# Performance work log

Measured on AMD Instinct MI355X. Metric: run time of the kernel, lower is better.

Reference implementation:

```python
import jax, jax.numpy as jnp
import numpy as np

B, S, E_BERT = 64, 512, 768
H = 64        # GRU hidden per direction (hidden_dim=128 bidirectional)
T = 16        # num output tags
P = 32        # pos_num_tags = attention embed dim


def setup_inputs() -> dict:
    key = jax.random.key(0)
    ks = jax.random.split(key, 20)
    def n(k, shape, s=0.1):
        return jax.random.normal(k, shape, dtype=jnp.float32) * s
    return {
        "bert_embed": n(ks[0], (B, S, E_BERT), 1.0),
        "input2": n(ks[1], (B, S, P), 1.0),
        "targets": jax.random.randint(ks[2], (B, S), 0, T),
        # forward-direction GRU (torch layout: W_ih (3H,E), W_hh (3H,H))
        "Wih_f": n(ks[3], (3 * H, E_BERT)), "Whh_f": n(ks[4], (3 * H, H)),
        "bih_f": n(ks[5], (3 * H,)), "bhh_f": n(ks[6], (3 * H,)),
        # backward-direction GRU
        "Wih_b": n(ks[7], (3 * H, E_BERT)), "Whh_b": n(ks[8], (3 * H, H)),
        "bih_b": n(ks[9], (3 * H,)), "bhh_b": n(ks[10], (3 * H,)),
        # dense (no bias): (2H -> T)
        "Wdense": n(ks[11], (2 * H, T)),
        # single-head MultiheadAttention over pos features
        "in_proj_w": n(ks[12], (3 * P, P)), "in_proj_b": n(ks[13], (3 * P,)),
        "out_proj_w": n(ks[14], (P, P)), "out_proj_b": n(ks[15], (P,)),
        # fusion linear (no bias): (T+P -> T)
        "Wfuse": n(ks[16], (T + P, T)),
        # CRF params
        "crf_start": n(ks[17], (T,)), "crf_end": n(ks[18], (T,)),
        "crf_trans": n(ks[19], (T, T)),
    }


def _gru_dir(x, Wih, Whh, bih, bhh, reverse):
    # x: (B,S,E) -> outputs (B,S,H); torch GRU cell math.
    xp = jnp.einsum('bse,ge->bsg', x, Wih) + bih      # precompute input gates (B,S,3H)
    xp = jnp.swapaxes(xp, 0, 1)                        # (S,B,3H)
    h0 = jnp.zeros((x.shape[0], Whh.shape[1]), x.dtype)
    def step(h, xt):
        gh = h @ Whh.T + bhh
        xr, xz, xn = jnp.split(xt, 3, axis=-1)
        hr, hz, hn = jnp.split(gh, 3, axis=-1)
        r = jax.nn.sigmoid(xr + hr)
        z = jax.nn.sigmoid(xz + hz)
        nw = jnp.tanh(xn + r * hn)
        h = (1.0 - z) * nw + z * h
        return h, h
    _, ys = jax.lax.scan(step, h0, xp, reverse=reverse)
    return jnp.swapaxes(ys, 0, 1)                      # (B,S,H)


def _forward(bert_embed, input2, targets,
             Wih_f, Whh_f, bih_f, bhh_f,
             Wih_b, Whh_b, bih_b, bhh_b,
             Wdense, in_proj_w, in_proj_b, out_proj_w, out_proj_b,
             Wfuse, crf_start, crf_end, crf_trans):
    # Bi-GRU over frozen BERT embeddings
    fwd = _gru_dir(bert_embed, Wih_f, Whh_f, bih_f, bhh_f, False)
    bwd = _gru_dir(bert_embed, Wih_b, Whh_b, bih_b, bhh_b, True)
    lstm_out = jnp.concatenate([fwd, bwd], axis=-1)    # (B,S,2H)
    dense = lstm_out @ Wdense                          # (B,S,T)

    # single-head self-attention on POS features (torch MultiheadAttention)
    qkv = input2 @ in_proj_w.T + in_proj_b
    q, k, v = jnp.split(qkv, 3, axis=-1)
    scores = jnp.einsum('bqd,bkd->bqk', q, k) / jnp.sqrt(jnp.float32(P))
    attn = jnp.einsum('bqk,bkd->bqd', jax.nn.softmax(scores, axis=-1), v)
    attn = attn @ out_proj_w.T + out_proj_b            # (B,S,P)

    # fusion -> emissions
    emis = jnp.concatenate([dense, attn], axis=-1) @ Wfuse  # (B,S,T)

    # CRF NLL (torchcrf, full mask, reduction='mean')
    em_tags = jnp.take_along_axis(emis, targets[..., None], axis=2)[..., 0]  # (B,S)
    numerator = (crf_start[targets[:, 0]]
                 + em_tags.sum(axis=-1)
                 + crf_trans[targets[:, :-1], targets[:, 1:]].sum(axis=-1)
                 + crf_end[targets[:, -1]])

    def step(score, em_t):  # score (B,T), em_t (B,T)
        nxt = jax.nn.logsumexp(score[:, :, None] + crf_trans[None] + em_t[:, None, :], axis=1)
        return nxt, None
    score0 = crf_start[None] + emis[:, 0]
    scoreF, _ = jax.lax.scan(step, score0, jnp.swapaxes(emis[:, 1:], 0, 1))
    denominator = jax.nn.logsumexp(scoreF + crf_end[None], axis=1)

    return jnp.mean(denominator - numerator)  # -mean(log_likelihood)


def reference(bert_embed, input2, targets,
              Wih_f, Whh_f, bih_f, bhh_f,
              Wih_b, Whh_b, bih_b, bhh_b,
              Wdense, in_proj_w, in_proj_b, out_proj_w, out_proj_b,
              Wfuse, crf_start, crf_end, crf_trans):
    return _forward(bert_embed, input2, targets,
                    Wih_f, Whh_f, bih_f, bhh_f,
                    Wih_b, Whh_b, bih_b, bhh_b,
                    Wdense, in_proj_w, in_proj_b, out_proj_w, out_proj_b,
                    Wfuse, crf_start, crf_end, crf_trans)
```

## Files before the change

### kernel.cpp

```cpp
#include <hip/hip_runtime.h>

#define Bn 64
#define Sn 512
#define EB 768
#define Hn 64
#define G3 192
#define Tn 16
#define Pn 32

__device__ __forceinline__ float sigmoidf_(float x) { return 1.f / (1.f + __expf(-x)); }
__device__ __forceinline__ float tanhf_(float x) { return 1.f - 2.f / (__expf(2.f * x) + 1.f); }

__device__ __forceinline__ unsigned short f2bf(float x) {
  union { float f; unsigned u; } v; v.f = x;
  unsigned r = v.u + 0x7fff + ((v.u >> 16) & 1);
  return (unsigned short)(r >> 16);
}

typedef __attribute__((ext_vector_type(8))) short short8;
typedef __attribute__((ext_vector_type(4))) float f32x4;

__global__ __launch_bounds__(256) void mega_a(const float* __restrict__ A,
                                              const float* __restrict__ Wf,
                                              const float* __restrict__ Wb,
                                              const float* __restrict__ bf,
                                              const float* __restrict__ bb,
                                              float* __restrict__ C,
                                              const float* __restrict__ in2,
                                              const float* __restrict__ Wqkv,
                                              const float* __restrict__ bqkv,
                                              float* __restrict__ qb,
                                              float* __restrict__ kb,
                                              float* __restrict__ vb,
                                              const float* __restrict__ Wdense,
                                              const float* __restrict__ Wfuse,
                                              float* __restrict__ wcomb) {
  __shared__ __align__(16) char smem[20864];
  const int gblk = blockIdx.x;
  const int tid = threadIdx.x;
  if (gblk < 768) {
    unsigned short* As = (unsigned short*)smem;
    unsigned short* Bs = As + 128 * 40;
    const int xcd = gblk & 7;
    const int slot = gblk >> 3;
    const int lin = xcd * 96 + slot;
    const int m_tile = lin / 3;
    const int n_tile = lin % 3;
    const int n0 = n_tile * 128;
    const int m0 = m_tile * 128;
    const int wv = tid >> 6;
    const int lane = tid & 63;
    const int wm = (wv >> 1) * 64, wn = (wv & 1) * 64;
    const int fr = lane & 15, fq = lane >> 4;
    const int srow = tid >> 1;
    const int shalf = (tid & 1) * 16;
    const int bcol = n0 + srow;
    const float* Wrow = (bcol < G3) ? (Wf + (size_t)bcol * EB) : (Wb + (size_t)(bcol - G3) * EB);
    const float* Arow = A + (size_t)(m0 + srow) * EB;
    f32x4 acc[4][4];
#pragma unroll
    for (int i = 0; i < 4; ++i)
#pragma unroll
      for (int j = 0; j < 4; ++j) acc[i][j] = (f32x4){0.f, 0.f, 0.f, 0.f};
    for (int k0 = 0; k0 < EB; k0 += 32) {
      float4 a0 = *(const float4*)&Arow[k0 + shalf + 0];
      float4 a1 = *(const float4*)&Arow[k0 + shalf + 4];
      float4 a2 = *(const float4*)&Arow[k0 + shalf + 8];
      float4 a3 = *(const float4*)&Arow[k0 + shalf + 12];
      float4 b0 = *(const float4*)&Wrow[k0 + shalf + 0];
      float4 b1 = *(const float4*)&Wrow[k0 + shalf + 4];
      float4 b2 = *(const float4*)&Wrow[k0 + shalf + 8];
      float4 b3 = *(const float4*)&Wrow[k0 + shalf + 12];
      __syncthreads();
      short8 pa, pb;
      pa[0] = f2bf(a0.x); pa[1] = f2bf(a0.y); pa[2] = f2bf(a0.z); pa[3] = f2bf(a0.w);
      pa[4] = f2bf(a1.x); pa[5] = f2bf(a1.y); pa[6] = f2bf(a1.z); pa[7] = f2bf(a1.w);
      *(short8*)&As[srow * 40 + shalf] = pa;
      pa[0] = f2bf(a2.x); pa[1] = f2bf(a2.y); pa[2] = f2bf(a2.z); pa[3] = f2bf(a2.w);
      pa[4] = f2bf(a3.x); pa[5] = f2bf(a3.y); pa[6] = f2bf(a3.z); pa[7] = f2bf(a3.w);
      *(short8*)&As[srow * 40 + shalf + 8] = pa;
      pb[0] = f2bf(b0.x); pb[1] = f2bf(b0.y); pb[2] = f2bf(b0.z); pb[3] = f2bf(b0.w);
      pb[4] = f2bf(b1.x); pb[5] = f2bf(b1.y); pb[6] = f2bf(b1.z); pb[7] = f2bf(b1.w);
      *(short8*)&Bs[srow * 40 + shalf] = pb;
      pb[0] = f2bf(b2.x); pb[1] = f2bf(b2.y); pb[2] = f2bf(b2.z); pb[3] = f2bf(b2.w);
      pb[4] = f2bf(b3.x); pb[5] = f2bf(b3.y); pb[6] = f2bf(b3.z); pb[7] = f2bf(b3.w);
      *(short8*)&Bs[srow * 40 + shalf + 8] = pb;
      __syncthreads();
      short8 af[4], bfv[4];
#pragma unroll
      for (int i = 0; i < 4; ++i) af[i] = *(short8*)&As[(wm + i * 16 + fr) * 40 + fq * 8];
#pragma unroll
      for (int j = 0; j < 4; ++j) bfv[j] = *(short8*)&Bs[(wn + j * 16 + fr) * 40 + fq * 8];
#pragma unroll
      for (int i = 0; i < 4; ++i)
#pragma unroll
        for (int j = 0; j < 4; ++j)
          acc[i][j] = __builtin_amdgcn_mfma_f32_16x16x32_bf16(af[i], bfv[j], acc[i][j], 0, 0, 0);
    }
#pragma unroll
    for (int j = 0; j < 4; ++j) {
      int col = n0 + wn + j * 16 + fr;
      float bias = (col < G3) ? bf[col] : bb[col - G3];
#pragma unroll
      for (int i = 0; i < 4; ++i) {
        int rowb = m0 + wm + i * 16 + fq * 4;
#pragma unroll
        for (int rg = 0; rg < 4; ++rg)
          C[(size_t)(rowb + rg) * 384 + col] = acc[i][j][rg] + bias;
      }
    }
  } else if (gblk < 896) {
    float* Ws = (float*)smem;
    float* bs = Ws + 96 * 32;
    for (int i = tid; i < 96 * 32; i += 256) Ws[i] = Wqkv[i];
    if (tid < 96) bs[tid] = bqkv[tid];
    __syncthreads();
    const int idx = (gblk - 768) * 256 + tid;
    float x[32];
#pragma unroll
    for (int d4 = 0; d4 < 8; ++d4) {
      float4 v = *(const float4*)&in2[(size_t)idx * 32 + d4 * 4];
      x[d4 * 4 + 0] = v.x; x[d4 * 4 + 1] = v.y; x[d4 * 4 + 2] = v.z; x[d4 * 4 + 3] = v.w;
    }
    float* const dsts[3] = {qb, kb, vb};
#pragma unroll
    for (int p = 0; p < 3; ++p) {
      float a[32];
#pragma unroll
      for (int j = 0; j < 32; ++j) {
        float s = bs[p * 32 + j];
#pragma unroll
        for (int d = 0; d < 32; ++d) s += x[d] * Ws[(p * 32 + j) * 32 + d];
        a[j] = s;
      }
      float* dst = dsts[p];
#pragma unroll
      for (int j4 = 0; j4 < 8; ++j4) {
        float4 o = {a[j4 * 4 + 0], a[j4 * 4 + 1], a[j4 * 4 + 2], a[j4 * 4 + 3]};
        *(float4*)&dst[(size_t)idx * 32 + j4 * 4] = o;
      }
    }
  } else {
    int e = (gblk - 896) * 256 + tid;
    int i = e >> 4, j = e & 15;
    float a = 0.f;
#pragma unroll
    for (int c = 0; c < 16; ++c) a += Wdense[i * 16 + c] * Wfuse[c * 16 + j];
    wcomb[e] = a;
  }
}

__global__ __launch_bounds__(256, 1) void mega_b(const float* __restrict__ C,
                                                 const float* __restrict__ Whh_f,
                                                 const float* __restrict__ bhh_f,
                                                 const float* __restrict__ Whh_b,
                                                 const float* __restrict__ bhh_b,
                                                 float* __restrict__ out,
                                                 const float* __restrict__ qb,
                                                 const float* __restrict__ kb,
                                                 const float* __restrict__ vb,
                                                 float* __restrict__ part) {
  __shared__ __align__(16) char smem[33280];
  const int tid = threadIdx.x;
  if (blockIdx.x < 128) {
    float* xs = (float*)smem;
    float* hbuf = xs + 32 * 192;
    float* obuf = hbuf + 128;
    const int wg = blockIdx.x;
    const int rev = (wg >= Bn) ? 1 : 0;
    const int b = wg & (Bn - 1);
    const int w = tid >> 6;
    const int lane = tid & 63;
    const int r = lane >> 2;
    const int kc = lane & 3;
    const int row = 16 * w + r;
    const int k0 = 16 * kc;
    const float* Whh = rev ? Whh_b : Whh_f;
    const float* bhh = rev ? bhh_b : bhh_f;
    const int colBase = rev ? G3 : 0;
    const int dirOff = rev ? Hn : 0;
    float4 wv[3][4];
#pragma unroll
    for (int g = 0; g < 3; ++g)
#pragma unroll
      for (int q = 0; q < 4; ++q) {
        wv[g][q] = *(const float4*)&Whh[(size_t)(g * 64 + row) * 64 + k0 + 4 * q];
        asm volatile("" : "+v"(wv[g][q].x), "+v"(wv[g][q].y), "+v"(wv[g][q].z), "+v"(wv[g][q].w));
      }
    const float brr = bhh[row], bzz = bhh[64 + row], bnn = bhh[128 + row];
    if (tid < 64) { hbuf[tid] = 0.f; hbuf[64 + tid] = 0.f; }
    float h = 0.f;
    for (int c = 0; c < 16; ++c) {
      const int cstart = c * 32;
      if (c > 0) {
#pragma unroll
        for (int i = 0; i < 2; ++i) {
          int f = tid + 256 * i;
          int s = f >> 4;
          int c4 = (f & 15) << 2;
          int tp = cstart - 32 + s;
          int orow = rev ? (Sn - 1 - tp) : tp;
          *(float4*)&out[(size_t)(b * Sn + orow) * 128 + dirOff + c4] = *(const float4*)&obuf[s * 64 + c4];
        }
      }
      float4 st[6];
#pragma unroll
      for (int i = 0; i < 6; ++i) {
        int f = tid + 256 * i;
        int s = f / 48;
        int c4 = (f % 48) << 2;
        int t = cstart + s;
        int grow = rev ? (Sn - 1 - t) : t;
        st[i] = *(const float4*)&C[(size_t)(b * Sn + grow) * 384 + colBase + c4];
      }
#pragma unroll
      for (int i = 0; i < 6; ++i) {
        int f = tid + 256 * i;
        int s = f / 48;
        int c4 = (f % 48) << 2;
        *(float4*)&xs[s * 192 + c4] = st[i];
      }
      __syncthreads();
      float xr = xs[row], xz = xs[64 + row], xn = xs[128 + row];
      for (int s = 0; s < 32; ++s) {
        const int t = cstart + s;
        const int p = t & 1;
        float4 ha = *(const float4*)&hbuf[p * 64 + k0 + 0];
        float4 hb = *(const float4*)&hbuf[p * 64 + k0 + 4];
        float4 hc = *(const float4*)&hbuf[p * 64 + k0 + 8];
        float4 hd = *(const float4*)&hbuf[p * 64 + k0 + 12];
        float nxr = 0.f, nxz = 0.f, nxn = 0.f;
        if (s + 1 < 32) {
          const float* xq = &xs[(s + 1) * 192];
          nxr = xq[row]; nxz = xq[64 + row]; nxn = xq[128 + row];
        }
        float dr, dz, dn;
        {
          float4 wa, wbv, wc, wd;
          wa = wv[0][0]; wbv = wv[0][1]; wc = wv[0][2]; wd = wv[0][3];
          dr = (wa.x * ha.x + wa.y * ha.y + wa.z * ha.z + wa.w * ha.w)
             + (wbv.x * hb.x + wbv.y * hb.y + wbv.z * hb.z + wbv.w * hb.w)
             + (wc.x * hc.x + wc.y * hc.y + wc.z * hc.z + wc.w * hc.w)
             + (wd.x * hd.x + wd.y * hd.y + wd.z * hd.z + wd.w * hd.w);
          wa = wv[1][0]; wbv = wv[1][1]; wc = wv[1][2]; wd = wv[1][3];
          dz = (wa.x * ha.x + wa.y * ha.y + wa.z * ha.z + wa.w * ha.w)
             + (wbv.x * hb.x + wbv.y * hb.y + wbv.z * hb.z + wbv.w * hb.w)
             + (wc.x * hc.x + wc.y * hc.y + wc.z * hc.z + wc.w * hc.w)
             + (wd.x * hd.x + wd.y * hd.y + wd.z * hd.z + wd.w * hd.w);
          wa = wv[2][0]; wbv = wv[2][1]; wc = wv[2][2]; wd = wv[2][3];
          dn = (wa.x * ha.x + wa.y * ha.y + wa.z * ha.z + wa.w * ha.w)
             + (wbv.x * hb.x + wbv.y * hb.y + wbv.z * hb.z + wbv.w * hb.w)
             + (wc.x * hc.x + wc.y * hc.y + wc.z * hc.z + wc.w * hc.w)
             + (wd.x * hd.x + wd.y * hd.y + wd.z * hd.z + wd.w * hd.w);
        }
        dr += __shfl_xor(dr, 1); dr += __shfl_xor(dr, 2);
        dz += __shfl_xor(dz, 1); dz += __shfl_xor(dz, 2);
        dn += __shfl_xor(dn, 1); dn += __shfl_xor(dn, 2);
        float rg = sigmoidf_(xr + brr + dr);
        float zg = sigmoidf_(xz + bzz + dz);
        float ng = tanhf_(xn + rg * (bnn + dn));
        h = (1.f - zg) * ng + zg * h;
        if (kc == 0) {
          hbuf[(p ^ 1) * 64 + row] = h;
          obuf[s * 64 + row] = h;
        }
        __syncthreads();
        xr = nxr; xz = nxz; xn = nxn;
      }
    }
#pragma unroll
    for (int i = 0; i < 2; ++i) {
      int f = tid + 256 * i;
      int s = f >> 4;
      int c4 = (f & 15) << 2;
      int tp = Sn - 32 + s;
      int orow = rev ? (Sn - 1 - tp) : tp;
      *(float4*)&out[(size_t)(b * Sn + orow) * 128 + dirOff + c4] = *(const float4*)&obuf[s * 64 + c4];
    }
  } else {
    float* Ks = (float*)smem;
    float* Vs = Ks + 128 * 32;
    const int blk = blockIdx.x - 128;
    const int b = blk >> 3;
    const int qhalf = (blk >> 2) & 1;
    const int split = blk & 3;
    const int k0 = split * 128;
#pragma unroll
    for (int i = 0; i < 4; ++i) {
      int f = tid + 256 * i;
      int row = f >> 3, col = (f & 7) * 4;
      *(float4*)&Ks[row * 32 + col] = *(const float4*)&kb[(size_t)(b * Sn + k0 + row) * 32 + col];
      *(float4*)&Vs[row * 32 + col] = *(const float4*)&vb[(size_t)(b * Sn + k0 + row) * 32 + col];
    }
    const int q = b * Sn + qhalf * 256 + tid;
    float qv[32];
#pragma unroll
    for (int d4 = 0; d4 < 8; ++d4) {
      float4 v = *(const float4*)&qb[(size_t)q * 32 + d4 * 4];
      qv[d4 * 4 + 0] = v.x; qv[d4 * 4 + 1] = v.y; qv[d4 * 4 + 2] = v.z; qv[d4 * 4 + 3] = v.w;
    }
    __syncthreads();
    const float scale = 0.17677669529663687f;
    float m = -1e30f, lsum = 0.f;
    float acc[32] = {};
    for (int kk = 0; kk < 128; ++kk) {
      const float4* kr = (const float4*)&Ks[kk * 32];
      float s = 0.f;
#pragma unroll
      for (int d4 = 0; d4 < 8; ++d4) {
        float4 kv = kr[d4];
        s += qv[d4 * 4 + 0] * kv.x + qv[d4 * 4 + 1] * kv.y + qv[d4 * 4 + 2] * kv.z + qv[d4 * 4 + 3] * kv.w;
      }
      s *= scale;
      float mn = fmaxf(m, s);
      float e1 = __expf(m - mn);
      float p = __expf(s - mn);
      lsum = lsum * e1 + p;
      const float4* vr = (const float4*)&Vs[kk * 32];
#pragma unroll
      for (int d4 = 0; d4 < 8; ++d4) {
        float4 vv = vr[d4];
        acc[d4 * 4 + 0] = acc[d4 * 4 + 0] * e1 + p * vv.x;
        acc[d4 * 4 + 1] = acc[d4 * 4 + 1] * e1 + p * vv.y;
        acc[d4 * 4 + 2] = acc[d4 * 4 + 2] * e1 + p * vv.z;
        acc[d4 * 4 + 3] = acc[d4 * 4 + 3] * e1 + p * vv.w;
      }
      m = mn;
    }
    float* rec = part + ((size_t)q * 4 + split) * 36;
#pragma unroll
    for (int d4 = 0; d4 < 8; ++d4) {
      float4 o = {acc[d4 * 4 + 0], acc[d4 * 4 + 1], acc[d4 * 4 + 2], acc[d4 * 4 + 3]};
      *(float4*)&rec[d4 * 4] = o;
    }
    rec[32] = m;
    rec[33] = lsum;
  }
}

__global__ __launch_bounds__(256) void attn_combine(const float* __restrict__ part,
                                                    const float* __restrict__ Wout,
                                                    const float* __restrict__ bout,
                                                    float* __restrict__ attn) {
  __shared__ float Ws[32 * 32];
  __shared__ float bs[32];
  const int tid = threadIdx.x;
  for (int i = tid; i < 1024; i += 256) Ws[i] = Wout[i];
  if (tid < 32) bs[tid] = bout[tid];
  __syncthreads();
  const int q = blockIdx.x * 256 + tid;
  const float* rec = part + (size_t)q * 4 * 36;
  float m0 = rec[32], m1 = rec[36 + 32], m2 = rec[72 + 32], m3 = rec[108 + 32];
  float M = fmaxf(fmaxf(m0, m1), fmaxf(m2, m3));
  float w0 = __expf(m0 - M), w1 = __expf(m1 - M), w2 = __expf(m2 - M), w3 = __expf(m3 - M);
  float L = rec[33] * w0 + rec[36 + 33] * w1 + rec[72 + 33] * w2 + rec[108 + 33] * w3;
  float inv = 1.f / L;
  float a[32];
#pragma unroll
  for (int d4 = 0; d4 < 8; ++d4) {
    float4 p0 = *(const float4*)&rec[d4 * 4];
    float4 p1 = *(const float4*)&rec[36 + d4 * 4];
    float4 p2 = *(const float4*)&rec[72 + d4 * 4];
    float4 p3 = *(const float4*)&rec[108 + d4 * 4];
    a[d4 * 4 + 0] = (p0.x * w0 + p1.x * w1 + p2.x * w2 + p3.x * w3) * inv;
    a[d4 * 4 + 1] = (p0.y * w0 + p1.y * w1 + p2.y * w2 + p3.y * w3) * inv;
    a[d4 * 4 + 2] = (p0.z * w0 + p1.z * w1 + p2.z * w2 + p3.z * w3) * inv;
    a[d4 * 4 + 3] = (p0.w * w0 + p1.w * w1 + p2.w * w2 + p3.w * w3) * inv;
  }
#pragma unroll
  for (int j = 0; j < 32; ++j) {
    float o = bs[j];
#pragma unroll
    for (int d = 0; d < 32; ++d) o += a[d] * Ws[j * 32 + d];
    attn[(size_t)q * 32 + j] = o;
  }
}

__global__ __launch_bounds__(256) void emis_kernel(const float* __restrict__ lstm,
                                                   const float* __restrict__ attn,
                                                   const float* __restrict__ wcomb,
                                                   const float* __restrict__ Wfuse,
                                                   float* __restrict__ emis) {
  __shared__ float Wc[128 * 16];
  __shared__ float Wf2[32 * 16];
  const int tid = threadIdx.x;
  for (int i = tid; i < 2048; i += 256) Wc[i] = wcomb[i];
  for (int i = tid; i < 512; i += 256) Wf2[i] = Wfuse[16 * 16 + i];
  __syncthreads();
  const int idx = blockIdx.x * 256 + tid;
  float acc[16] = {};
  for (int i = 0; i < 128; i += 4) {
    float4 lv = *(const float4*)&lstm[(size_t)idx * 128 + i];
    float ll[4] = {lv.x, lv.y, lv.z, lv.w};
#pragma unroll
    for (int u = 0; u < 4; ++u)
#pragma unroll
      for (int j = 0; j < 16; ++j) acc[j] += ll[u] * Wc[(i + u) * 16 + j];
  }
  for (int d = 0; d < 32; d += 4) {
    float4 av = *(const float4*)&attn[(size_t)idx * 32 + d];
    float aa[4] = {av.x, av.y, av.z, av.w};
#pragma unroll
    for (int u = 0; u < 4; ++u)
#pragma unroll
      for (int j = 0; j < 16; ++j) acc[j] += aa[u] * Wf2[(d + u) * 16 + j];
  }
#pragma unroll
  for (int j = 0; j < 16; j += 4) {
    float4 o = {acc[j], acc[j + 1], acc[j + 2], acc[j + 3]};
    *(float4*)&emis[(size_t)idx * 16 + j] = o;
  }
}

__global__ __launch_bounds__(256) void scan_kernel(const float* __restrict__ emis,
                                                   const float* __restrict__ ctrans,
                                                   float* __restrict__ scanbuf) {
  __shared__ __align__(16) float P[16 * 20];
  const int blk = blockIdx.x;
  const int b = blk >> 3;
  const int g = blk & 7;
  const int tid = threadIdx.x;
  const int i = tid >> 4;
  const int j = tid & 15;
  const int t0 = 1 + 64 * g;
  const int t1 = (64 + 64 * g < 511) ? (64 + 64 * g) : 511;
  float trk[16];
#pragma unroll
  for (int k = 0; k < 16; ++k) trk[k] = ctrans[k * 16 + j];
  P[i * 20 + j] = ctrans[i * 16 + j] + emis[((size_t)(b * Sn + t0)) * Tn + j];
  float em_next = emis[((size_t)(b * Sn + t0 + 1)) * Tn + j];
  __syncthreads();
  float out = 0.f;
  for (int t = t0 + 1; t <= t1; ++t) {
    float4 r0 = *(const float4*)&P[i * 20 + 0];
    float4 r1 = *(const float4*)&P[i * 20 + 4];
    float4 r2 = *(const float4*)&P[i * 20 + 8];
    float4 r3 = *(const float4*)&P[i * 20 + 12];
    float em_t = em_next;
    if (t + 1 <= t1) em_next = emis[((size_t)(b * Sn + t + 1)) * Tn + j];
    float wk[16];
    wk[0] = r0.x + trk[0]; wk[1] = r0.y + trk[1]; wk[2] = r0.z + trk[2]; wk[3] = r0.w + trk[3];
    wk[4] = r1.x + trk[4]; wk[5] = r1.y + trk[5]; wk[6] = r1.z + trk[6]; wk[7] = r1.w + trk[7];
    wk[8] = r2.x + trk[8]; wk[9] = r2.y + trk[9]; wk[10] = r2.z + trk[10]; wk[11] = r2.w + trk[11];
    wk[12] = r3.x + trk[12]; wk[13] = r3.y + trk[13]; wk[14] = r3.z + trk[14]; wk[15] = r3.w + trk[15];
    float m = wk[0];
#pragma unroll
    for (int k = 1; k < 16; ++k) m = fmaxf(m, wk[k]);
    float e = 0.f;
#pragma unroll
    for (int k = 0; k < 16; ++k) e += __expf(wk[k] - m);
    out = m + __logf(e) + em_t;
    __syncthreads();
    P[i * 20 + j] = out;
    __syncthreads();
  }
  scanbuf[((size_t)blk) * 256 + i * 16 + j] = P[i * 20 + j];
}

__global__ __launch_bounds__(64) void mega_e(const float* __restrict__ emis,
                                             const int* __restrict__ tgt,
                                             const float* __restrict__ cstart,
                                             const float* __restrict__ cend,
                                             const float* __restrict__ ctrans,
                                             const float* __restrict__ scanbuf,
                                             float* __restrict__ numer,
                                             float* __restrict__ denom) {
  if (blockIdx.x < 64) {
    const int b = blockIdx.x, l = threadIdx.x;
    float ssum = 0.f;
    for (int t = l; t < Sn; t += 64) {
      int tg = tgt[b * Sn + t];
      ssum += emis[(size_t)(b * Sn + t) * Tn + tg];
      if (t + 1 < Sn) {
        int tg2 = tgt[b * Sn + t + 1];
        ssum += ctrans[tg * Tn + tg2];
      }
    }
    if (l == 0) ssum += cstart[tgt[b * Sn]] + cend[tgt[b * Sn + Sn - 1]];
    for (int off = 32; off > 0; off >>= 1) ssum += __shfl_down(ssum, off);
    if (l == 0) numer[b] = ssum;
  } else {
    __shared__ __align__(16) float vbuf[16];
    const int b = blockIdx.x - 64;
    const int lane = threadIdx.x;
    const int j = lane & 15;
    float v = cstart[j] + emis[(size_t)(b * Sn) * Tn + j];
    if (lane < 16) vbuf[j] = v;
    for (int g = 0; g < 8; ++g) {
      float4 v0 = *(const float4*)&vbuf[0];
      float4 v1 = *(const float4*)&vbuf[4];
      float4 v2 = *(const float4*)&vbuf[8];
      float4 v3 = *(const float4*)&vbuf[12];
      const float* P = scanbuf + ((size_t)(b * 8 + g)) * 256;
      float wk[16];
#pragma unroll
      for (int k = 0; k < 16; ++k) wk[k] = P[k * 16 + j];
      wk[0] += v0.x; wk[1] += v0.y; wk[2] += v0.z; wk[3] += v0.w;
      wk[4] += v1.x; wk[5] += v1.y; wk[6] += v1.z; wk[7] += v1.w;
      wk[8] += v2.x; wk[9] += v2.y; wk[10] += v2.z; wk[11] += v2.w;
      wk[12] += v3.x; wk[13] += v3.y; wk[14] += v3.z; wk[15] += v3.w;
      float m = wk[0];
#pragma unroll
      for (int k = 1; k < 16; ++k) m = fmaxf(m, wk[k]);
      float e = 0.f;
#pragma unroll
      for (int k = 0; k < 16; ++k) e += __expf(wk[k] - m);
      float nv = m + __logf(e);
      if (lane < 16) vbuf[j] = nv;
    }
    float f = vbuf[j] + cend[j];
    float m = f;
    m = fmaxf(m, __shfl_xor(m, 1));
    m = fmaxf(m, __shfl_xor(m, 2));
    m = fmaxf(m, __shfl_xor(m, 4));
    m = fmaxf(m, __shfl_xor(m, 8));
    float e = __expf(f - m);
    e += __shfl_xor(e, 1);
    e += __shfl_xor(e, 2);
    e += __shfl_xor(e, 4);
    e += __shfl_xor(e, 8);
    if (lane == 0) denom[b] = m + __logf(e);
  }
}

__global__ __launch_bounds__(64) void final_kernel(const float* __restrict__ numer,
                                                   const float* __restrict__ denom,
                                                   float* __restrict__ out) {
  const int l = threadIdx.x;
  float d = denom[l] - numer[l];
  for (int off = 32; off > 0; off >>= 1) d += __shfl_down(d, off);
  if (l == 0) out[0] = d * (1.f / 64.f);
}

extern "C" void kernel_launch(void* const* d_in, const int* in_sizes, int n_in,
                              void* d_out, int out_size, void* d_ws, size_t ws_size,
                              hipStream_t stream) {
  (void)in_sizes; (void)n_in; (void)out_size; (void)ws_size;
  const float* bert = (const float*)d_in[0];
  const float* in2 = (const float*)d_in[1];
  const int* tgt = (const int*)d_in[2];
  const float* Wih_f = (const float*)d_in[3];
  const float* Whh_f = (const float*)d_in[4];
  const float* bih_f = (const float*)d_in[5];
  const float* bhh_f = (const float*)d_in[6];
  const float* Wih_b = (const float*)d_in[7];
  const float* Whh_b = (const float*)d_in[8];
  const float* bih_b = (const float*)d_in[9];
  const float* bhh_b = (const float*)d_in[10];
  const float* Wdense = (const float*)d_in[11];
  const float* in_proj_w = (const float*)d_in[12];
  const float* in_proj_b = (const float*)d_in[13];
  const float* out_proj_w = (const float*)d_in[14];
  const float* out_proj_b = (const float*)d_in[15];
  const float* Wfuse = (const float*)d_in[16];
  const float* cstart = (const float*)d_in[17];
  const float* cend = (const float*)d_in[18];
  const float* ctrans = (const float*)d_in[19];

  float* ws = (float*)d_ws;
  float* C = ws;
  float* lstm = C + (size_t)Bn * Sn * 384;
  float* qb = lstm + (size_t)Bn * Sn * 2 * Hn;
  float* kb = qb + (size_t)Bn * Sn * Pn;
  float* vb = kb + (size_t)Bn * Sn * Pn;
  float* attn = vb + (size_t)Bn * Sn * Pn;
  float* emis = attn + (size_t)Bn * Sn * Pn;
  float* wcomb = emis + (size_t)Bn * Sn * Tn;
  float* numer = wcomb + 2048;
  float* denom = numer + Bn;
  float* part = denom + Bn;
  float* scanbuf = part + (size_t)32768 * 4 * 36;

  mega_a<<<904, 256, 0, stream>>>(bert, Wih_f, Wih_b, bih_f, bih_b, C,
                                  in2, in_proj_w, in_proj_b, qb, kb, vb,
                                  Wdense, Wfuse, wcomb);
  mega_b<<<640, 256, 0, stream>>>(C, Whh_f, bhh_f, Whh_b, bhh_b, lstm,
                                  qb, kb, vb, part);
  attn_combine<<<Bn * Sn / 256, 256, 0, stream>>>(part, out_proj_w, out_proj_b, attn);
  emis_kernel<<<Bn * Sn / 256, 256, 0, stream>>>(lstm, attn, wcomb, Wfuse, emis);
  scan_kernel<<<Bn * 8, 256, 0, stream>>>(emis, ctrans, scanbuf);
  mega_e<<<128, 64, 0, stream>>>(emis, tgt, cstart, cend, ctrans, scanbuf, numer, denom);
  final_kernel<<<1, 64, 0, stream>>>(numer, denom, (float*)d_out);
}
```

Before: 545.3 us.

## Pre-convert GEMM operands to bf16 and double-buffer LDS tiles in input projection

Result: no change. 541.8 us (-0.7%).

```diff
diff --git a/kernel.cpp b/kernel.cpp
--- a/kernel.cpp
+++ b/kernel.cpp
@@ -20,9 +20,29 @@
 typedef __attribute__((ext_vector_type(8))) short short8;
 typedef __attribute__((ext_vector_type(4))) float f32x4;
 
-__global__ __launch_bounds__(256) void mega_a(const float* __restrict__ A,
-                                              const float* __restrict__ Wf,
-                                              const float* __restrict__ Wb,
+__global__ __launch_bounds__(256) void convert_kernel(const float* __restrict__ bert,
+                                                      const float* __restrict__ Wf,
+                                                      const float* __restrict__ Wb,
+                                                      unsigned short* __restrict__ Abf,
+                                                      unsigned short* __restrict__ Wbf) {
+  const int blk = blockIdx.x;
+  const float* src;
+  unsigned short* dst;
+  size_t base;
+  if (blk < 12288) { src = bert; dst = Abf; base = (size_t)blk * 2048; }
+  else if (blk < 12360) { src = Wf; dst = Wbf; base = (size_t)(blk - 12288) * 2048; }
+  else { src = Wb; dst = Wbf + 147456; base = (size_t)(blk - 12360) * 2048; }
+  size_t e = base + (size_t)threadIdx.x * 8;
+  float4 v0 = *(const float4*)&src[e];
+  float4 v1 = *(const float4*)&src[e + 4];
+  short8 o;
+  o[0] = f2bf(v0.x); o[1] = f2bf(v0.y); o[2] = f2bf(v0.z); o[3] = f2bf(v0.w);
+  o[4] = f2bf(v1.x); o[5] = f2bf(v1.y); o[6] = f2bf(v1.z); o[7] = f2bf(v1.w);
+  *(short8*)&dst[e] = o;
+}
+
+__global__ __launch_bounds__(256) void mega_a(const unsigned short* __restrict__ Abf,
+                                              const unsigned short* __restrict__ Wbf,
                                               const float* __restrict__ bf,
                                               const float* __restrict__ bb,
                                               float* __restrict__ C,
@@ -35,12 +55,14 @@
                                               const float* __restrict__ Wdense,
                                               const float* __restrict__ Wfuse,
                                               float* __restrict__ wcomb) {
-  __shared__ __align__(16) char smem[20864];
+  __shared__ __align__(16) char smem[40960];
   const int gblk = blockIdx.x;
   const int tid = threadIdx.x;
   if (gblk < 768) {
-    unsigned short* As = (unsigned short*)smem;
-    unsigned short* Bs = As + 128 * 40;
+    unsigned short* As0 = (unsigned short*)smem;
+    unsigned short* Bs0 = As0 + 128 * 40;
+    unsigned short* As1 = Bs0 + 128 * 40;
+    unsigned short* Bs1 = As1 + 128 * 40;
     const int xcd = gblk & 7;
     const int slot = gblk >> 3;
     const int lin = xcd * 96 + slot;
@@ -54,38 +76,32 @@
     const int fr = lane & 15, fq = lane >> 4;
     const int srow = tid >> 1;
     const int shalf = (tid & 1) * 16;
-    const int bcol = n0 + srow;
-    const float* Wrow = (bcol < G3) ? (Wf + (size_t)bcol * EB) : (Wb + (size_t)(bcol - G3) * EB);
-    const float* Arow = A + (size_t)(m0 + srow) * EB;
+    const unsigned short* Arow = Abf + (size_t)(m0 + srow) * EB;
+    const unsigned short* Brow = Wbf + (size_t)(n0 + srow) * EB;
     f32x4 acc[4][4];
 #pragma unroll
     for (int i = 0; i < 4; ++i)
 #pragma unroll
       for (int j = 0; j < 4; ++j) acc[i][j] = (f32x4){0.f, 0.f, 0.f, 0.f};
-    for (int k0 = 0; k0 < EB; k0 += 32) {
-      float4 a0 = *(const float4*)&Arow[k0 + shalf + 0];
-      float4 a1 = *(const float4*)&Arow[k0 + shalf + 4];
-      float4 a2 = *(const float4*)&Arow[k0 + shalf + 8];
-      float4 a3 = *(const float4*)&Arow[k0 + shalf + 12];
-      float4 b0 = *(const float4*)&Wrow[k0 + shalf + 0];
-      float4 b1 = *(const float4*)&Wrow[k0 + shalf + 4];
-      float4 b2 = *(const float4*)&Wrow[k0 + shalf + 8];
-      float4 b3 = *(const float4*)&Wrow[k0 + shalf + 12];
+    short8 ra0 = *(const short8*)&Arow[shalf];
+    short8 ra1 = *(const short8*)&Arow[shalf + 8];
+    short8 rb0 = *(const short8*)&Brow[shalf];
+    short8 rb1 = *(const short8*)&Brow[shalf + 8];
+    for (int kt = 0; kt < 24; ++kt) {
+      unsigned short* As = (kt & 1) ? As1 : As0;
+      unsigned short* Bs = (kt & 1) ? Bs1 : Bs0;
+      *(short8*)&As[srow * 40 + shalf] = ra0;
+      *(short8*)&As[srow * 40 + shalf + 8] = ra1;
+      *(short8*)&Bs[srow * 40 + shalf] = rb0;
+      *(short8*)&Bs[srow * 40 + shalf + 8] = rb1;
       __syncthreads();
-      short8 pa, pb;
-      pa[0] = f2bf(a0.x); pa[1] = f2bf(a0.y); pa[2] = f2bf(a0.z); pa[3] = f2bf(a0.w);
-      pa[4] = f2bf(a1.x); pa[5] = f2bf(a1.y); pa[6] = f2bf(a1.z); pa[7] = f2bf(a1.w);
-      *(short8*)&As[srow * 40 + shalf] = pa;
-      pa[0] = f2bf(a2.x); pa[1] = f2bf(a2.y); pa[2] = f2bf(a2.z); pa[3] = f2bf(a2.w);
-      pa[4] = f2bf(a3.x); pa[5] = f2bf(a3.y); pa[6] = f2bf(a3.z); pa[7] = f2bf(a3.w);
-      *(short8*)&As[srow * 40 + shalf + 8] = pa;
-      pb[0] = f2bf(b0.x); pb[1] = f2bf(b0.y); pb[2] = f2bf(b0.z); pb[3] = f2bf(b0.w);
-      pb[4] = f2bf(b1.x); pb[5] = f2bf(b1.y); pb[6] = f2bf(b1.z); pb[7] = f2bf(b1.w);
-      *(short8*)&Bs[srow * 40 + shalf] = pb;
-      pb[0] = f2bf(b2.x); pb[1] = f2bf(b2.y); pb[2] = f2bf(b2.z); pb[3] = f2bf(b2.w);
-      pb[4] = f2bf(b3.x); pb[5] = f2bf(b3.y); pb[6] = f2bf(b3.z); pb[7] = f2bf(b3.w);
-      *(short8*)&Bs[srow * 40 + shalf + 8] = pb;
-      __syncthreads();
+      if (kt + 1 < 24) {
+        const int k0 = (kt + 1) * 32;
+        ra0 = *(const short8*)&Arow[k0 + shalf];
+        ra1 = *(const short8*)&Arow[k0 + shalf + 8];
+        rb0 = *(const short8*)&Brow[k0 + shalf];
+        rb1 = *(const short8*)&Brow[k0 + shalf + 8];
+      }
       short8 af[4], bfv[4];
 #pragma unroll
       for (int i = 0; i < 4; ++i) af[i] = *(short8*)&As[(wm + i * 16 + fr) * 40 + fq * 8];
@@ -559,19 +575,23 @@
 
   float* ws = (float*)d_ws;
   float* C = ws;
-  float* lstm = C + (size_t)Bn * Sn * 384;
-  float* qb = lstm + (size_t)Bn * Sn * 2 * Hn;
-  float* kb = qb + (size_t)Bn * Sn * Pn;
-  float* vb = kb + (size_t)Bn * Sn * Pn;
-  float* attn = vb + (size_t)Bn * Sn * Pn;
-  float* emis = attn + (size_t)Bn * Sn * Pn;
-  float* wcomb = emis + (size_t)Bn * Sn * Tn;
+  float* lstm = C + (size_t)12582912;
+  float* qb = lstm + (size_t)4194304;
+  float* kb = qb + (size_t)1048576;
+  float* vb = kb + (size_t)1048576;
+  float* emis = vb + (size_t)1048576;
+  float* wcomb = emis + (size_t)524288;
   float* numer = wcomb + 2048;
-  float* denom = numer + Bn;
-  float* part = denom + Bn;
-  float* scanbuf = part + (size_t)32768 * 4 * 36;
-
-  mega_a<<<904, 256, 0, stream>>>(bert, Wih_f, Wih_b, bih_f, bih_b, C,
+  float* denom = numer + 64;
+  float* region = denom + 64;
+  unsigned short* Abf = (unsigned short*)region;
+  float* part = region;
+  float* scanbuf = part + (size_t)4718592;
+  float* attn = scanbuf + (size_t)131072;
+  unsigned short* Wbf = (unsigned short*)(region + (size_t)12582912);
+
+  convert_kernel<<<12432, 256, 0, stream>>>(bert, Wih_f, Wih_b, Abf, Wbf);
+  mega_a<<<904, 256, 0, stream>>>(Abf, Wbf, bih_f, bih_b, C,
                                   in2, in_proj_w, in_proj_b, qb, kb, vb,
                                   Wdense, Wfuse, wcomb);
   mega_b<<<640, 256, 0, stream>>>(C, Whh_f, bhh_f, Whh_b, bhh_b, lstm,
```
